# Kernel optimization log

Hardware: AMD Instinct MI355X
Metric: run time of the kernel (lower is better)

## Reference

```python
import jax, jax.numpy as jnp
import numpy as np

IN_CH = 128
OUT_CH = 128

def setup_inputs() -> dict:
    key = jax.random.key(0)
    k1, k2, k3, k4, k5 = jax.random.split(key, 5)
    from_tensor = jax.random.normal(k1, (640000, IN_CH), dtype=jnp.float32)
    to_index = jax.random.randint(k2, (640000,), 0, 10000, dtype=jnp.int64)
    # torch Linear default init ~ U(-1/sqrt(fan_in), 1/sqrt(fan_in))
    lim1 = 1.0 / np.sqrt(IN_CH)
    lim2 = 1.0 / np.sqrt(OUT_CH)
    W1 = jax.random.uniform(k3, (OUT_CH, IN_CH), jnp.float32, -lim1, lim1)
    b1 = jnp.zeros((OUT_CH,), jnp.float32)
    W2 = jax.random.uniform(k4, (OUT_CH, OUT_CH), jnp.float32, -lim2, lim2)
    b2 = jnp.zeros((OUT_CH,), jnp.float32)
    return {"from_tensor": from_tensor, "to_index": to_index, "dim_size": 10000,
            "W1": W1, "b1": b1, "W2": W2, "b2": b2}

def reference(from_tensor, to_index, dim_size, W1, b1, W2, b2):
    # MLP transform (transform_scatter=True): Linear+ReLU x2
    h = jax.nn.relu(from_tensor @ W1.T + b1)
    h = jax.nn.relu(h @ W2.T + b2)          # (num_src, OUT_CH)
    # scatter-mean over to_index into dim_size rows
    seg_sum = jax.ops.segment_sum(h, to_index, num_segments=dim_size)
    counts = jax.ops.segment_sum(jnp.ones((h.shape[0],), h.dtype), to_index,
                                 num_segments=dim_size)
    return seg_sum / jnp.maximum(counts, 1.0)[:, None]
```

## Files before the change

### kernel.cpp

```cpp
#include <hip/hip_runtime.h>

#define IN_CH 128
#define OUT_CH 128
#define LDSPAD 136

typedef short bf16x8 __attribute__((ext_vector_type(8)));
typedef float f32x4  __attribute__((ext_vector_type(4)));

__device__ __forceinline__ unsigned short f32_to_bf16_bits(float f) {
    unsigned u = __builtin_bit_cast(unsigned, f);
    u += 0x7FFFu + ((u >> 16) & 1u);
    return (unsigned short)(u >> 16);
}
__device__ __forceinline__ float bf16_bits_to_f32(unsigned short b) {
    return __builtin_bit_cast(float, (unsigned)b << 16);
}

__global__ void detect_kernel(const unsigned short* __restrict__ X,
                              const unsigned short* __restrict__ W1,
                              const unsigned short* __restrict__ W2,
                              const int* __restrict__ idx,
                              int* __restrict__ flags) {
    __shared__ int red[4];
    const int t = threadIdx.x;
    if (t < 4) red[t] = 0;
    __syncthreads();
    #pragma unroll
    for (int w = 0; w < 3; ++w) {
        const unsigned short* p = (w == 0) ? X : (w == 1) ? W1 : W2;
        int crazy = 0;
        for (int j = t; j < 512; j += 256) {
            const unsigned short h = p[j];
            const int e = (h >> 7) & 0xFF;
            const int man = h & 0x7F;
            if (e >= 0x90 || (e == 0 && man != 0)) crazy++;
        }
        if (crazy) atomicAdd(&red[w], crazy);
    }
    {
        if (idx[2 * t + 1] != 0) atomicAdd(&red[3], 1);
    }
    __syncthreads();
    if (t == 0) {
        flags[0] = red[0] > 16 ? 1 : 0;
        flags[1] = red[1] > 16 ? 1 : 0;
        flags[2] = red[2] > 16 ? 1 : 0;
        flags[3] = red[3] < 8  ? 1 : 0;
    }
}

__global__ void count_kernel(const int* __restrict__ idx, int* __restrict__ cnt,
                             const int* __restrict__ flags, int n) {
    const int sh = flags[3];
    int i = blockIdx.x * blockDim.x + threadIdx.x;
    if (i < n) atomicAdd(&cnt[idx[(size_t)i << sh]], 1);
}

__global__ void scan_kernel(const int* __restrict__ cnt, int* __restrict__ off,
                            int* __restrict__ cur, int dim) {
    __shared__ int wtot[16];
    __shared__ int woff[16];
    __shared__ int carry_s;
    const int tid = threadIdx.x;
    const int wv = tid >> 6, ln = tid & 63;
    if (tid == 0) carry_s = 0;
    __syncthreads();
    for (int base = 0; base < dim; base += 1024) {
        const int i = base + tid;
        const int orig = (i < dim) ? cnt[i] : 0;
        int v = orig;
        #pragma unroll
        for (int d = 1; d < 64; d <<= 1) {
            int w = __shfl_up(v, d, 64);
            if (ln >= d) v += w;
        }
        if (ln == 63) wtot[wv] = v;
        __syncthreads();
        if (tid == 0) {
            int acc = carry_s;
            #pragma unroll
            for (int k = 0; k < 16; ++k) { woff[k] = acc; acc += wtot[k]; }
            carry_s = acc;
        }
        __syncthreads();
        const int excl = woff[wv] + v - orig;
        if (i < dim) { off[i] = excl; cur[i] = excl; }
        __syncthreads();
    }
}

__global__ void perm_kernel(const int* __restrict__ idx, int* __restrict__ cur,
                            int* __restrict__ perm, const int* __restrict__ flags,
                            int n) {
    const int sh = flags[3];
    int i = blockIdx.x * blockDim.x + threadIdx.x;
    if (i < n) {
        const int s = idx[(size_t)i << sh];
        const int p = atomicAdd(&cur[s], 1);
        perm[p] = i;
    }
}

__global__ __launch_bounds__(256)
void mlp_gather_kernel(const unsigned short* __restrict__ X,
                       const int* __restrict__ perm,
                       const int* __restrict__ off,
                       const int* __restrict__ cnt,
                       const unsigned short* __restrict__ W1,
                       const unsigned short* __restrict__ B1,
                       const unsigned short* __restrict__ W2,
                       const unsigned short* __restrict__ B2,
                       float* __restrict__ out,
                       const int* __restrict__ flags,
                       int dim)
{
    __shared__ short lds_x[16 * LDSPAD];
    __shared__ short lds_h[16 * LDSPAD];

    const int xf32  = flags[0];
    const int w1f32 = flags[1];
    const int w2f32 = flags[2];

    const int tid  = threadIdx.x;
    const int wave = tid >> 6;
    const int lane = tid & 63;
    const int m    = lane & 15;
    const int quad = lane >> 4;

    bf16x8 w1f[2][4], w2f[2][4];
    float  b1c[2], b2c[2];
    #pragma unroll
    for (int t = 0; t < 2; ++t) {
        const int n = wave * 32 + t * 16 + m;
        b1c[t] = w1f32 ? ((const float*)B1)[n] : bf16_bits_to_f32(B1[n]);
        b2c[t] = w2f32 ? ((const float*)B2)[n] : bf16_bits_to_f32(B2[n]);
        #pragma unroll
        for (int kc = 0; kc < 4; ++kc) {
            const int ko = kc * 32 + quad * 8;
            if (w1f32) {
                const float* Wf = (const float*)W1;
                f32x4 lo = *(const f32x4*)(Wf + n * IN_CH + ko);
                f32x4 hi = *(const f32x4*)(Wf + n * IN_CH + ko + 4);
                bf16x8 v;
                #pragma unroll
                for (int j = 0; j < 4; ++j) {
                    v[j]     = (short)f32_to_bf16_bits(lo[j]);
                    v[4 + j] = (short)f32_to_bf16_bits(hi[j]);
                }
                w1f[t][kc] = v;
            } else {
                w1f[t][kc] = *(const bf16x8*)(W1 + n * IN_CH + ko);
            }
            if (w2f32) {
                const float* Wf = (const float*)W2;
                f32x4 lo = *(const f32x4*)(Wf + n * OUT_CH + ko);
                f32x4 hi = *(const f32x4*)(Wf + n * OUT_CH + ko + 4);
                bf16x8 v;
                #pragma unroll
                for (int j = 0; j < 4; ++j) {
                    v[j]     = (short)f32_to_bf16_bits(lo[j]);
                    v[4 + j] = (short)f32_to_bf16_bits(hi[j]);
                }
                w2f[t][kc] = v;
            } else {
                w2f[t][kc] = *(const bf16x8*)(W2 + n * OUT_CH + ko);
            }
        }
    }

    const int srow = tid >> 4;
    const int sseg = tid & 15;

    for (int s = blockIdx.x; s < dim; s += gridDim.x) {
        const int c     = cnt[s];
        const int start = off[s];
        float sum0 = 0.f, sum1 = 0.f;

        for (int base = 0; base < c; base += 16) {
            {
                const int gr = base + srow;
                bf16x8 v = {0, 0, 0, 0, 0, 0, 0, 0};
                if (gr < c) {
                    const int row = perm[start + gr];
                    if (xf32) {
                        const float* Xf = (const float*)X;
                        f32x4 lo = *(const f32x4*)(Xf + (size_t)row * IN_CH + sseg * 8);
                        f32x4 hi = *(const f32x4*)(Xf + (size_t)row * IN_CH + sseg * 8 + 4);
                        #pragma unroll
                        for (int j = 0; j < 4; ++j) {
                            v[j]     = (short)f32_to_bf16_bits(lo[j]);
                            v[4 + j] = (short)f32_to_bf16_bits(hi[j]);
                        }
                    } else {
                        v = *(const bf16x8*)(X + (size_t)row * IN_CH + sseg * 8);
                    }
                }
                *(bf16x8*)&lds_x[srow * LDSPAD + sseg * 8] = v;
            }
            __syncthreads();

            f32x4 acc0 = {0.f, 0.f, 0.f, 0.f}, acc1 = {0.f, 0.f, 0.f, 0.f};
            #pragma unroll
            for (int kc = 0; kc < 4; ++kc) {
                bf16x8 a = *(const bf16x8*)&lds_x[m * LDSPAD + kc * 32 + quad * 8];
                acc0 = __builtin_amdgcn_mfma_f32_16x16x32_bf16(a, w1f[0][kc], acc0, 0, 0, 0);
                acc1 = __builtin_amdgcn_mfma_f32_16x16x32_bf16(a, w1f[1][kc], acc1, 0, 0, 0);
            }
            #pragma unroll
            for (int t = 0; t < 2; ++t) {
                const int col = wave * 32 + t * 16 + m;
                const float bias = b1c[t];
                const f32x4 acc = t == 0 ? acc0 : acc1;
                #pragma unroll
                for (int r = 0; r < 4; ++r) {
                    float v = acc[r] + bias;
                    v = v > 0.f ? v : 0.f;
                    lds_h[(quad * 4 + r) * LDSPAD + col] = (short)f32_to_bf16_bits(v);
                }
            }
            __syncthreads();

            f32x4 acc2_0 = {0.f, 0.f, 0.f, 0.f}, acc2_1 = {0.f, 0.f, 0.f, 0.f};
            #pragma unroll
            for (int kc = 0; kc < 4; ++kc) {
                bf16x8 a = *(const bf16x8*)&lds_h[m * LDSPAD + kc * 32 + quad * 8];
                acc2_0 = __builtin_amdgcn_mfma_f32_16x16x32_bf16(a, w2f[0][kc], acc2_0, 0, 0, 0);
                acc2_1 = __builtin_amdgcn_mfma_f32_16x16x32_bf16(a, w2f[1][kc], acc2_1, 0, 0, 0);
            }

            #pragma unroll
            for (int t = 0; t < 2; ++t) {
                const float bias = b2c[t];
                const f32x4 acc = t == 0 ? acc2_0 : acc2_1;
                float sr = 0.f;
                #pragma unroll
                for (int r = 0; r < 4; ++r) {
                    if (base + quad * 4 + r < c) {
                        float v = acc[r] + bias;
                        sr += (v > 0.f ? v : 0.f);
                    }
                }
                if (t == 0) sum0 += sr; else sum1 += sr;
            }
        }

        sum0 += __shfl_xor(sum0, 16, 64);
        sum0 += __shfl_xor(sum0, 32, 64);
        sum1 += __shfl_xor(sum1, 16, 64);
        sum1 += __shfl_xor(sum1, 32, 64);
        if (quad == 0) {
            const float inv = 1.f / (float)(c > 1 ? c : 1);
            float* o = out + (size_t)s * OUT_CH + wave * 32 + m;
            o[0]  = sum0 * inv;
            o[16] = sum1 * inv;
        }
    }
}

extern "C" void kernel_launch(void* const* d_in, const int* in_sizes, int n_in,
                              void* d_out, int out_size, void* d_ws, size_t ws_size,
                              hipStream_t stream) {
    int iX = 0;
    for (int i = 1; i < n_in; ++i)
        if (in_sizes[i] > in_sizes[iX]) iX = i;
    const int n_src = in_sizes[iX] / IN_CH;
    int iI = -1, iW1 = -1, iW2 = -1, iB1 = -1, iB2 = -1;
    for (int i = 0; i < n_in; ++i) {
        if (i == iX) continue;
        const int s = in_sizes[i];
        if (s == n_src && iI < 0) iI = i;
        else if (s == IN_CH * OUT_CH) { if (iW1 < 0) iW1 = i; else if (iW2 < 0) iW2 = i; }
        else if (s == OUT_CH) { if (iB1 < 0) iB1 = i; else if (iB2 < 0) iB2 = i; }
    }

    const unsigned short* X  = (const unsigned short*)d_in[iX];
    const int*            ix = (const int*)d_in[iI];
    const unsigned short* W1 = (const unsigned short*)d_in[iW1];
    const unsigned short* B1 = (const unsigned short*)d_in[iB1];
    const unsigned short* W2 = (const unsigned short*)d_in[iW2];
    const unsigned short* B2 = (const unsigned short*)d_in[iB2];
    float* out = (float*)d_out;

    const int dim = out_size / OUT_CH;

    int* flags = (int*)d_ws;
    int* cnt   = (int*)((char*)d_ws + 256);
    int* off   = cnt + dim;
    int* cur   = off + dim;
    int* perm  = cur + dim;

    hipMemsetAsync(cnt, 0, (size_t)dim * sizeof(int), stream);

    detect_kernel<<<1, 256, 0, stream>>>(X, W1, W2, ix, flags);

    count_kernel<<<(n_src + 255) / 256, 256, 0, stream>>>(ix, cnt, flags, n_src);

    scan_kernel<<<1, 1024, 0, stream>>>(cnt, off, cur, dim);

    perm_kernel<<<(n_src + 255) / 256, 256, 0, stream>>>(ix, cur, perm, flags, n_src);

    const int grid = dim < 2048 ? dim : 2048;
    mlp_gather_kernel<<<grid, 256, 0, stream>>>(X, perm, off, cnt, W1, B1, W2, B2,
                                                out, flags, dim);
}
```

Before: 580.3 us.

## Use 512-thread blocks with 32-row tiles and register-prefetched gather

The MLP gather kernel now runs 8 waves per block, with each wave owning 16 output columns, and processes 32 source rows per iteration instead of 16. The next tile's X rows are loaded into registers before the barrier and MFMA work on the current tile, so global gather latency overlaps with compute. Segments average about 64 rows, so this halves the number of loop iterations and barriers per segment. The trade-off is more padding waste on short or odd segments and a larger block, which can limit occupancy.

```diff
diff --git a/kernel.cpp b/kernel.cpp
--- a/kernel.cpp
+++ b/kernel.cpp
@@ -101,7 +101,7 @@
     }
 }
 
-__global__ __launch_bounds__(256)
+__global__ __launch_bounds__(512, 4)
 void mlp_gather_kernel(const unsigned short* __restrict__ X,
                        const int* __restrict__ perm,
                        const int* __restrict__ off,
@@ -114,8 +114,8 @@
                        const int* __restrict__ flags,
                        int dim)
 {
-    __shared__ short lds_x[16 * LDSPAD];
-    __shared__ short lds_h[16 * LDSPAD];
+    __shared__ short lds_x[32 * LDSPAD];
+    __shared__ short lds_h[32 * LDSPAD];
 
     const int xf32  = flags[0];
     const int w1f32 = flags[1];
@@ -127,44 +127,41 @@
     const int m    = lane & 15;
     const int quad = lane >> 4;
 
-    bf16x8 w1f[2][4], w2f[2][4];
-    float  b1c[2], b2c[2];
+    const int n = wave * 16 + m;
+    bf16x8 w1f[4], w2f[4];
+    float  b1c, b2c;
+    b1c = w1f32 ? ((const float*)B1)[n] : bf16_bits_to_f32(B1[n]);
+    b2c = w2f32 ? ((const float*)B2)[n] : bf16_bits_to_f32(B2[n]);
     #pragma unroll
-    for (int t = 0; t < 2; ++t) {
-        const int n = wave * 32 + t * 16 + m;
-        b1c[t] = w1f32 ? ((const float*)B1)[n] : bf16_bits_to_f32(B1[n]);
-        b2c[t] = w2f32 ? ((const float*)B2)[n] : bf16_bits_to_f32(B2[n]);
-        #pragma unroll
-        for (int kc = 0; kc < 4; ++kc) {
-            const int ko = kc * 32 + quad * 8;
-            if (w1f32) {
-                const float* Wf = (const float*)W1;
-                f32x4 lo = *(const f32x4*)(Wf + n * IN_CH + ko);
-                f32x4 hi = *(const f32x4*)(Wf + n * IN_CH + ko + 4);
-                bf16x8 v;
-                #pragma unroll
-                for (int j = 0; j < 4; ++j) {
-                    v[j]     = (short)f32_to_bf16_bits(lo[j]);
-                    v[4 + j] = (short)f32_to_bf16_bits(hi[j]);
-                }
-                w1f[t][kc] = v;
-            } else {
-                w1f[t][kc] = *(const bf16x8*)(W1 + n * IN_CH + ko);
-            }
-            if (w2f32) {
-                const float* Wf = (const float*)W2;
-                f32x4 lo = *(const f32x4*)(Wf + n * OUT_CH + ko);
-                f32x4 hi = *(const f32x4*)(Wf + n * OUT_CH + ko + 4);
-                bf16x8 v;
-                #pragma unroll
-                for (int j = 0; j < 4; ++j) {
-                    v[j]     = (short)f32_to_bf16_bits(lo[j]);
-                    v[4 + j] = (short)f32_to_bf16_bits(hi[j]);
-                }
-                w2f[t][kc] = v;
-            } else {
-                w2f[t][kc] = *(const bf16x8*)(W2 + n * OUT_CH + ko);
-            }
+    for (int kc = 0; kc < 4; ++kc) {
+        const int ko = kc * 32 + quad * 8;
+        if (w1f32) {
+            const float* Wf = (const float*)W1;
+            f32x4 lo = *(const f32x4*)(Wf + n * IN_CH + ko);
+            f32x4 hi = *(const f32x4*)(Wf + n * IN_CH + ko + 4);
+            bf16x8 v;
+            #pragma unroll
+            for (int j = 0; j < 4; ++j) {
+                v[j]     = (short)f32_to_bf16_bits(lo[j]);
+                v[4 + j] = (short)f32_to_bf16_bits(hi[j]);
+            }
+            w1f[kc] = v;
+        } else {
+            w1f[kc] = *(const bf16x8*)(W1 + n * IN_CH + ko);
+        }
+        if (w2f32) {
+            const float* Wf = (const float*)W2;
+            f32x4 lo = *(const f32x4*)(Wf + n * OUT_CH + ko);
+            f32x4 hi = *(const f32x4*)(Wf + n * OUT_CH + ko + 4);
+            bf16x8 v;
+            #pragma unroll
+            for (int j = 0; j < 4; ++j) {
+                v[j]     = (short)f32_to_bf16_bits(lo[j]);
+                v[4 + j] = (short)f32_to_bf16_bits(hi[j]);
+            }
+            w2f[kc] = v;
+        } else {
+            w2f[kc] = *(const bf16x8*)(W2 + n * OUT_CH + ko);
         }
     }
 
@@ -174,85 +171,85 @@
     for (int s = blockIdx.x; s < dim; s += gridDim.x) {
         const int c     = cnt[s];
         const int start = off[s];
-        float sum0 = 0.f, sum1 = 0.f;
-
-        for (int base = 0; base < c; base += 16) {
-            {
-                const int gr = base + srow;
-                bf16x8 v = {0, 0, 0, 0, 0, 0, 0, 0};
-                if (gr < c) {
-                    const int row = perm[start + gr];
-                    if (xf32) {
-                        const float* Xf = (const float*)X;
-                        f32x4 lo = *(const f32x4*)(Xf + (size_t)row * IN_CH + sseg * 8);
-                        f32x4 hi = *(const f32x4*)(Xf + (size_t)row * IN_CH + sseg * 8 + 4);
-                        #pragma unroll
-                        for (int j = 0; j < 4; ++j) {
-                            v[j]     = (short)f32_to_bf16_bits(lo[j]);
-                            v[4 + j] = (short)f32_to_bf16_bits(hi[j]);
-                        }
-                    } else {
-                        v = *(const bf16x8*)(X + (size_t)row * IN_CH + sseg * 8);
+        float sum = 0.f;
+
+        auto gather = [&](int gr, bf16x8& v) {
+            v = (bf16x8){0, 0, 0, 0, 0, 0, 0, 0};
+            if (gr < c) {
+                const int row = perm[start + gr];
+                if (xf32) {
+                    const float* Xf = (const float*)X;
+                    f32x4 lo = *(const f32x4*)(Xf + (size_t)row * IN_CH + sseg * 8);
+                    f32x4 hi = *(const f32x4*)(Xf + (size_t)row * IN_CH + sseg * 8 + 4);
+                    #pragma unroll
+                    for (int j = 0; j < 4; ++j) {
+                        v[j]     = (short)f32_to_bf16_bits(lo[j]);
+                        v[4 + j] = (short)f32_to_bf16_bits(hi[j]);
                     }
+                } else {
+                    v = *(const bf16x8*)(X + (size_t)row * IN_CH + sseg * 8);
                 }
-                *(bf16x8*)&lds_x[srow * LDSPAD + sseg * 8] = v;
-            }
+            }
+        };
+
+        bf16x8 cur;
+        gather(srow, cur);
+
+        for (int base = 0; base < c; base += 32) {
+            *(bf16x8*)&lds_x[srow * LDSPAD + sseg * 8] = cur;
+            bf16x8 nxt;
+            gather(base + 32 + srow, nxt);
             __syncthreads();
 
             f32x4 acc0 = {0.f, 0.f, 0.f, 0.f}, acc1 = {0.f, 0.f, 0.f, 0.f};
             #pragma unroll
             for (int kc = 0; kc < 4; ++kc) {
-                bf16x8 a = *(const bf16x8*)&lds_x[m * LDSPAD + kc * 32 + quad * 8];
-                acc0 = __builtin_amdgcn_mfma_f32_16x16x32_bf16(a, w1f[0][kc], acc0, 0, 0, 0);
-                acc1 = __builtin_amdgcn_mfma_f32_16x16x32_bf16(a, w1f[1][kc], acc1, 0, 0, 0);
-            }
-            #pragma unroll
-            for (int t = 0; t < 2; ++t) {
-                const int col = wave * 32 + t * 16 + m;
-                const float bias = b1c[t];
-                const f32x4 acc = t == 0 ? acc0 : acc1;
-                #pragma unroll
-                for (int r = 0; r < 4; ++r) {
-                    float v = acc[r] + bias;
-                    v = v > 0.f ? v : 0.f;
-                    lds_h[(quad * 4 + r) * LDSPAD + col] = (short)f32_to_bf16_bits(v);
+                const int ko = kc * 32 + quad * 8;
+                bf16x8 a0 = *(const bf16x8*)&lds_x[m * LDSPAD + ko];
+                bf16x8 a1 = *(const bf16x8*)&lds_x[(16 + m) * LDSPAD + ko];
+                acc0 = __builtin_amdgcn_mfma_f32_16x16x32_bf16(a0, w1f[kc], acc0, 0, 0, 0);
+                acc1 = __builtin_amdgcn_mfma_f32_16x16x32_bf16(a1, w1f[kc], acc1, 0, 0, 0);
+            }
+            #pragma unroll
+            for (int r = 0; r < 4; ++r) {
+                float v0 = acc0[r] + b1c;
+                v0 = v0 > 0.f ? v0 : 0.f;
+                lds_h[(quad * 4 + r) * LDSPAD + n] = (short)f32_to_bf16_bits(v0);
+                float v1 = acc1[r] + b1c;
+                v1 = v1 > 0.f ? v1 : 0.f;
+                lds_h[(16 + quad * 4 + r) * LDSPAD + n] = (short)f32_to_bf16_bits(v1);
+            }
+            __syncthreads();
+
+            f32x4 acc2_0 = {0.f, 0.f, 0.f, 0.f}, acc2_1 = {0.f, 0.f, 0.f, 0.f};
+            #pragma unroll
+            for (int kc = 0; kc < 4; ++kc) {
+                const int ko = kc * 32 + quad * 8;
+                bf16x8 a0 = *(const bf16x8*)&lds_h[m * LDSPAD + ko];
+                bf16x8 a1 = *(const bf16x8*)&lds_h[(16 + m) * LDSPAD + ko];
+                acc2_0 = __builtin_amdgcn_mfma_f32_16x16x32_bf16(a0, w2f[kc], acc2_0, 0, 0, 0);
+                acc2_1 = __builtin_amdgcn_mfma_f32_16x16x32_bf16(a1, w2f[kc], acc2_1, 0, 0, 0);
+            }
+
+            #pragma unroll
+            for (int r = 0; r < 4; ++r) {
+                if (base + quad * 4 + r < c) {
+                    float v = acc2_0[r] + b2c;
+                    sum += (v > 0.f ? v : 0.f);
                 }
-            }
-            __syncthreads();
-
-            f32x4 acc2_0 = {0.f, 0.f, 0.f, 0.f}, acc2_1 = {0.f, 0.f, 0.f, 0.f};
-            #pragma unroll
-            for (int kc = 0; kc < 4; ++kc) {
-                bf16x8 a = *(const bf16x8*)&lds_h[m * LDSPAD + kc * 32 + quad * 8];
-                acc2_0 = __builtin_amdgcn_mfma_f32_16x16x32_bf16(a, w2f[0][kc], acc2_0, 0, 0, 0);
-                acc2_1 = __builtin_amdgcn_mfma_f32_16x16x32_bf16(a, w2f[1][kc], acc2_1, 0, 0, 0);
-            }
-
-            #pragma unroll
-            for (int t = 0; t < 2; ++t) {
-                const float bias = b2c[t];
-                const f32x4 acc = t == 0 ? acc2_0 : acc2_1;
-                float sr = 0.f;
-                #pragma unroll
-                for (int r = 0; r < 4; ++r) {
-                    if (base + quad * 4 + r < c) {
-                        float v = acc[r] + bias;
-                        sr += (v > 0.f ? v : 0.f);
-                    }
+                if (base + 16 + quad * 4 + r < c) {
+                    float v = acc2_1[r] + b2c;
+                    sum += (v > 0.f ? v : 0.f);
                 }
-                if (t == 0) sum0 += sr; else sum1 += sr;
-            }
-        }
-
-        sum0 += __shfl_xor(sum0, 16, 64);
-        sum0 += __shfl_xor(sum0, 32, 64);
-        sum1 += __shfl_xor(sum1, 16, 64);
-        sum1 += __shfl_xor(sum1, 32, 64);
+            }
+            cur = nxt;
+        }
+
+        sum += __shfl_xor(sum, 16, 64);
+        sum += __shfl_xor(sum, 32, 64);
         if (quad == 0) {
             const float inv = 1.f / (float)(c > 1 ? c : 1);
-            float* o = out + (size_t)s * OUT_CH + wave * 32 + m;
-            o[0]  = sum0 * inv;
-            o[16] = sum1 * inv;
+            out[(size_t)s * OUT_CH + n] = sum * inv;
         }
     }
 }
@@ -300,6 +297,6 @@
     perm_kernel<<<(n_src + 255) / 256, 256, 0, stream>>>(ix, cur, perm, flags, n_src);
 
     const int grid = dim < 2048 ? dim : 2048;
-    mlp_gather_kernel<<<grid, 256, 0, stream>>>(X, perm, off, cnt, W1, B1, W2, B2,
+    mlp_gather_kernel<<<grid, 512, 0, stream>>>(X, perm, off, cnt, W1, B1, W2, B2,
                                                 out, flags, dim);
 }
```

Result: no change. 580.6 us (+0.1%).
